# Performance work log

Hardware: AMD Instinct MI355X
Metric: run time of the kernel (lower is better)

## Reference

```python
import jax, jax.numpy as jnp
import numpy as np

INPUT_SIZE = 64
HIDDEN = 1024
SEQ_LEN = 256
BATCH = 128
TARGET_LEN = 96


def lstm_cell(x, h, c, Wih, Whh, bih, bhh):
    # x: [B, in], h/c: [B, H]; torch gate order: i, f, g, o
    z = x @ Wih.T + h @ Whh.T + bih + bhh  # [B, 4H]
    i, f, g, o = jnp.split(z, 4, axis=-1)
    c_new = jax.nn.sigmoid(f) * c + jax.nn.sigmoid(i) * jnp.tanh(g)
    h_new = jax.nn.sigmoid(o) * jnp.tanh(c_new)
    return h_new, c_new


def setup_inputs() -> dict:
    key = jax.random.key(0)
    ks = jax.random.split(key, 12)
    s_in = 1.0 / np.sqrt(HIDDEN)  # torch LSTM init scale ~ U(-1/sqrt(H), 1/sqrt(H))
    def u(k, shape):
        return jax.random.uniform(k, shape, jnp.float32, -s_in, s_in)
    return {
        "input_batch": jax.random.normal(ks[0], (SEQ_LEN, BATCH, INPUT_SIZE), jnp.float32),
        "target_batch": jax.random.normal(ks[1], (TARGET_LEN, BATCH, INPUT_SIZE), jnp.float32),
        "enc_Wih": u(ks[2], (4 * HIDDEN, INPUT_SIZE)),
        "enc_Whh": u(ks[3], (4 * HIDDEN, HIDDEN)),
        "enc_bih": u(ks[4], (4 * HIDDEN,)),
        "enc_bhh": u(ks[5], (4 * HIDDEN,)),
        "dec_Wih": u(ks[6], (4 * HIDDEN, INPUT_SIZE)),
        "dec_Whh": u(ks[7], (4 * HIDDEN, HIDDEN)),
        "dec_bih": u(ks[8], (4 * HIDDEN,)),
        "dec_bhh": u(ks[9], (4 * HIDDEN,)),
        "lin_W": u(ks[10], (INPUT_SIZE, HIDDEN)),
        "lin_b": u(ks[11], (INPUT_SIZE,)),
    }


def reference(input_batch, target_batch, enc_Wih, enc_Whh, enc_bih, enc_bhh,
              dec_Wih, dec_Whh, dec_bih, dec_bhh, lin_W, lin_b):
    B = input_batch.shape[1]
    h0 = jnp.zeros((B, HIDDEN), input_batch.dtype)
    c0 = jnp.zeros((B, HIDDEN), input_batch.dtype)

    # ---- encoder: LSTM over seq_len ----
    def enc_step(carry, x_t):
        h, c = carry
        h, c = lstm_cell(x_t, h, c, enc_Wih, enc_Whh, enc_bih, enc_bhh)
        return (h, c), None
    (h_enc, c_enc), _ = jax.lax.scan(enc_step, (h0, c0), input_batch)

    # ---- decoder: recursive (no teacher forcing), target_len steps ----
    def dec_step(carry, _):
        x, h, c = carry
        h, c = lstm_cell(x, h, c, dec_Wih, dec_Whh, dec_bih, dec_bhh)
        y = h @ lin_W.T + lin_b  # [B, input_size]
        return (y, h, c), y
    x0 = input_batch[-1]  # [B, input_size]
    _, outputs = jax.lax.scan(dec_step, (x0, h_enc, c_enc), None, length=TARGET_LEN)
    return outputs  # [target_len, B, input_size]
```

## Files before the change

### kernel.cpp

```cpp
#include <hip/hip_runtime.h>
#include <stdint.h>

#define IN    64
#define H     1024
#define G4    4096
#define BATCH 128
#define SEQ   256
#define TLEN  96
#define KCAT  1088
#define NSTEP (SEQ + TLEN)
#define NBLK  256
#define HPAD  1032

typedef __attribute__((ext_vector_type(8))) short bf16x8;
typedef __attribute__((ext_vector_type(4))) float f32x4;

__device__ __forceinline__ unsigned short f2bf(float f) {
  union { float f; uint32_t u; } v; v.f = f;
  uint32_t u = v.u;
  return (unsigned short)((u + 0x7fffu + ((u >> 16) & 1u)) >> 16);
}

__device__ __forceinline__ void gload_lds16_sc0(const unsigned short* g, unsigned short* l) {
  __builtin_amdgcn_global_load_lds((const __attribute__((address_space(1))) unsigned int*)g,
                                   (__attribute__((address_space(3))) unsigned int*)l, 16, 0, 1);
}

__global__ void k_convert(const float* __restrict__ src, unsigned short* __restrict__ dst, int n) {
  int i = blockIdx.x * blockDim.x + threadIdx.x;
  int stride = gridDim.x * blockDim.x;
  for (; i < n; i += stride) dst[i] = f2bf(src[i]);
}

__global__ void k_pack(const float* __restrict__ Wih, const float* __restrict__ Whh,
                       const float* __restrict__ bih, const float* __restrict__ bhh,
                       unsigned short* __restrict__ Wcat, float* __restrict__ bcat) {
  int p = blockIdx.x;
  int j = p >> 2, g = p & 3;
  int r = g * H + j;
  for (int c = threadIdx.x; c < KCAT; c += blockDim.x) {
    float v = (c < IN) ? Wih[r * IN + c] : Whh[r * H + (c - IN)];
    Wcat[(size_t)p * KCAT + c] = f2bf(v);
  }
  if (threadIdx.x == 0) bcat[p] = bih[r] + bhh[r];
}

__global__ void k_deceff(const float* __restrict__ Wih, const float* __restrict__ Whh,
                         const float* __restrict__ bih, const float* __restrict__ bhh,
                         const float* __restrict__ lin, const float* __restrict__ linb,
                         unsigned short* __restrict__ Weff, float* __restrict__ beff) {
  int p = blockIdx.x;
  int j = p >> 2, g = p & 3;
  int r = g * H + j;
  __shared__ float wr[IN];
  if (threadIdx.x < IN) wr[threadIdx.x] = Wih[r * IN + threadIdx.x];
  __syncthreads();
  for (int k = threadIdx.x; k < H; k += blockDim.x) {
    float acc = Whh[(size_t)r * H + k];
    #pragma unroll 8
    for (int i = 0; i < IN; ++i) acc += wr[i] * lin[(size_t)i * H + k];
    Weff[(size_t)p * H + k] = f2bf(acc);
  }
  if (threadIdx.x == 0) {
    float s = bih[r] + bhh[r];
    for (int i = 0; i < IN; ++i) s += wr[i] * linb[i];
    beff[p] = s;
  }
}

__global__ __launch_bounds__(512, 2) void k_lstm(
    const unsigned short* __restrict__ xin,
    const unsigned short* __restrict__ Wenc,  const float* __restrict__ benc,
    const unsigned short* __restrict__ Wdec0, const float* __restrict__ bdec0,
    const unsigned short* __restrict__ Wdeff, const float* __restrict__ bdeff,
    unsigned short* __restrict__ hbuf, unsigned short* __restrict__ hhist,
    unsigned int* __restrict__ flags, unsigned int* __restrict__ tickets)
{
  extern __shared__ char smem[];
  unsigned short* hs = (unsigned short*)smem;
  __shared__ unsigned short ht[16][40];
  __shared__ int s_xcd, s_slot;
  const int tid  = threadIdx.x;
  const int lane = tid & 63;
  const int wave = tid >> 6;
  if (tid == 0) {
    unsigned x;
    asm volatile("s_getreg_b32 %0, hwreg(HW_REG_XCC_ID)" : "=s"(x));
    x &= 7;
    unsigned tk = __hip_atomic_fetch_add(&tickets[x], 1u, __ATOMIC_RELAXED, __HIP_MEMORY_SCOPE_AGENT);
    s_xcd = (int)x; s_slot = (int)(tk & 31);
  }
  __syncthreads();
  const int grp  = s_xcd;
  const int slot = s_slot;
  const int m0   = grp * 16;
  const int n0   = slot * 128;
  const int gw   = n0 + wave * 16;
  const int fm   = lane & 15;
  const int fku  = lane >> 4;
  const int fk   = fku * 8;
  const int unit = slot * 32 + wave * 4 + fku;
  const int hrow = tid >> 5;
  const int hcol = tid & 31;
  const unsigned int* myflags = flags + (size_t)grp * 32;

  bf16x8 B[34];
  float4 bias4;
  float cst = 0.f;
  int p = 0;
  for (int t = 0; t < NSTEP; ++t) {
    const bool is_enc = (t < SEQ);
    if (t == 0 || t == SEQ) {
      const unsigned short* W = (t == 0) ? Wenc : Wdec0;
      const unsigned short* wr = W + (size_t)(gw + fm) * KCAT + fk;
      #pragma unroll
      for (int kt = 0; kt < 32; ++kt) B[kt] = *(const bf16x8*)(wr + IN + kt * 32);
      B[32] = *(const bf16x8*)(wr);
      B[33] = *(const bf16x8*)(wr + 32);
    } else if (t == SEQ + 1) {
      const unsigned short* wr = Wdeff + (size_t)(gw + fm) * H + fk;
      #pragma unroll
      for (int kt = 0; kt < 32; ++kt) B[kt] = *(const bf16x8*)(wr + kt * 32);
    }
    if (t == 0 || t == SEQ || t == SEQ + 1) {
      const float* bptr = (t == 0) ? benc : (t == SEQ ? bdec0 : bdeff);
      bias4 = *(const float4*)&bptr[4 * unit];
    }
    const unsigned short* xsrc =
        is_enc ? xin + (size_t)t * BATCH * IN
               : (t == SEQ ? xin + (size_t)(SEQ - 1) * BATCH * IN : nullptr);
    if (t > 0) {
      const unsigned short* hb = hbuf + (size_t)p * BATCH * H + (size_t)m0 * H;
      #pragma unroll
      for (int j = 0; j < 4; ++j) {
        int row  = wave * 2 + (j >> 1);
        int half = (j & 1) * 512;
        gload_lds16_sc0(hb + (size_t)row * H + half + lane * 8, &hs[row * HPAD + half]);
      }
    }
    __syncthreads();
    f32x4 acc0 = {0.f, 0.f, 0.f, 0.f};
    f32x4 acc1 = {0.f, 0.f, 0.f, 0.f};
    if (t > 0) {
      const unsigned short* as = &hs[fm * HPAD + fk];
      #pragma unroll
      for (int kt = 0; kt < 32; kt += 2) {
        acc0 = __builtin_amdgcn_mfma_f32_16x16x32_bf16(B[kt],     *(const bf16x8*)(as + kt * 32),      acc0, 0, 0, 0);
        acc1 = __builtin_amdgcn_mfma_f32_16x16x32_bf16(B[kt + 1], *(const bf16x8*)(as + kt * 32 + 32), acc1, 0, 0, 0);
      }
    }
    if (xsrc) {
      const unsigned short* xa = xsrc + (size_t)(m0 + fm) * IN + fk;
      acc0 = __builtin_amdgcn_mfma_f32_16x16x32_bf16(B[32], *(const bf16x8*)(xa),      acc0, 0, 0, 0);
      acc1 = __builtin_amdgcn_mfma_f32_16x16x32_bf16(B[33], *(const bf16x8*)(xa + 32), acc1, 0, 0, 0);
    }
    {
      float zi = acc0[0] + acc1[0] + bias4.x;
      float zf = acc0[1] + acc1[1] + bias4.y;
      float zg = acc0[2] + acc1[2] + bias4.z;
      float zo = acc0[3] + acc1[3] + bias4.w;
      float gi = 1.f / (1.f + __expf(-zi));
      float gf = 1.f / (1.f + __expf(-zf));
      float gg = tanhf(zg);
      float go = 1.f / (1.f + __expf(-zo));
      float c  = gf * cst + gi * gg;
      cst = c;
      float h = go * tanhf(c);
      ht[fm][(wave << 2) + fku] = f2bf(h);
    }
    __syncthreads();
    {
      unsigned short hv = ht[hrow][hcol];
      size_t idx = (size_t)(m0 + hrow) * H + (size_t)slot * 32 + hcol;
      hbuf[(size_t)(1 - p) * BATCH * H + idx] = hv;
      if (!is_enc) hhist[(size_t)(t - SEQ) * BATCH * H + idx] = hv;
    }
    p ^= 1;
    if (t + 1 < NSTEP) {
      __syncthreads();
      if (tid == 0)
        __hip_atomic_store(&flags[grp * 32 + slot], (unsigned)(t + 1),
                           __ATOMIC_RELAXED, __HIP_MEMORY_SCOPE_AGENT);
      if (tid < 32) {
        while (__hip_atomic_load(&myflags[tid], __ATOMIC_RELAXED, __HIP_MEMORY_SCOPE_AGENT) < (unsigned)(t + 1))
          __builtin_amdgcn_s_sleep(1);
      }
      __syncthreads();
    }
  }
}

__global__ __launch_bounds__(256) void k_out(
    const unsigned short* __restrict__ hhist, const unsigned short* __restrict__ linb16,
    const float* __restrict__ linb, float* __restrict__ out)
{
  const int tid  = threadIdx.x;
  const int lane = tid & 63;
  const int wave = tid >> 6;
  const int fm   = lane & 15;
  const int fk   = (lane >> 4) * 8;
  const int R0   = blockIdx.x * 64 + wave * 16;
  f32x4 acc[4] = {{0.f,0.f,0.f,0.f},{0.f,0.f,0.f,0.f},{0.f,0.f,0.f,0.f},{0.f,0.f,0.f,0.f}};
  const unsigned short* ha = hhist + (size_t)(R0 + fm) * H + fk;
  #pragma unroll 2
  for (int kc = 0; kc < H; kc += 32) {
    bf16x8 a = *(const bf16x8*)(ha + kc);
    #pragma unroll
    for (int nq = 0; nq < 4; ++nq) {
      bf16x8 b = *(const bf16x8*)(linb16 + (size_t)(nq * 16 + fm) * H + fk + kc);
      acc[nq] = __builtin_amdgcn_mfma_f32_16x16x32_bf16(a, b, acc[nq], 0, 0, 0);
    }
  }
  #pragma unroll
  for (int nq = 0; nq < 4; ++nq) {
    int col = nq * 16 + fm;
    float bb = linb[col];
    #pragma unroll
    for (int j = 0; j < 4; ++j) {
      int R = R0 + (lane >> 4) * 4 + j;
      out[(size_t)R * IN + col] = acc[nq][j] + bb;
    }
  }
}

extern "C" void kernel_launch(void* const* d_in, const int* in_sizes, int n_in,
                              void* d_out, int out_size, void* d_ws, size_t ws_size,
                              hipStream_t stream) {
  const float* input_batch = (const float*)d_in[0];
  const float* eWih = (const float*)d_in[2];
  const float* eWhh = (const float*)d_in[3];
  const float* ebih = (const float*)d_in[4];
  const float* ebhh = (const float*)d_in[5];
  const float* dWih = (const float*)d_in[6];
  const float* dWhh = (const float*)d_in[7];
  const float* dbih = (const float*)d_in[8];
  const float* dbhh = (const float*)d_in[9];
  const float* linW = (const float*)d_in[10];
  const float* linb = (const float*)d_in[11];
  float* out = (float*)d_out;

  char* ws = (char*)d_ws;
  size_t off = 0;
  auto alloc = [&](size_t bytes) -> void* {
    void* pp = ws + off;
    off = (off + bytes + 255) & ~(size_t)255;
    return pp;
  };
  unsigned short* xin   = (unsigned short*)alloc((size_t)SEQ * BATCH * IN * 2);
  unsigned short* Wenc  = (unsigned short*)alloc((size_t)G4 * KCAT * 2);
  float*          benc  = (float*)         alloc((size_t)G4 * 4);
  unsigned short* Wdec0 = (unsigned short*)alloc((size_t)G4 * KCAT * 2);
  float*          bdec0 = (float*)         alloc((size_t)G4 * 4);
  unsigned short* Wdeff = (unsigned short*)alloc((size_t)G4 * H * 2);
  float*          bdeff = (float*)         alloc((size_t)G4 * 4);
  unsigned short* linbf = (unsigned short*)alloc((size_t)IN * H * 2);
  unsigned short* hbuf  = (unsigned short*)alloc((size_t)2 * BATCH * H * 2);
  unsigned short* hhist = (unsigned short*)alloc((size_t)TLEN * BATCH * H * 2);
  unsigned int*   flags = (unsigned int*)  alloc((size_t)8 * 32 * sizeof(unsigned));
  unsigned int*   tickets = (unsigned int*)alloc((size_t)8 * sizeof(unsigned));
  (void)ws_size; (void)in_sizes; (void)n_in; (void)out_size;

  hipMemsetAsync(flags, 0, (size_t)8 * 32 * sizeof(unsigned), stream);
  hipMemsetAsync(tickets, 0, (size_t)8 * sizeof(unsigned), stream);
  hipLaunchKernelGGL(k_convert, dim3(512), dim3(256), 0, stream, input_batch, xin, SEQ * BATCH * IN);
  hipLaunchKernelGGL(k_convert, dim3(64),  dim3(256), 0, stream, linW, linbf, IN * H);
  hipLaunchKernelGGL(k_pack,   dim3(G4), dim3(256), 0, stream, eWih, eWhh, ebih, ebhh, Wenc, benc);
  hipLaunchKernelGGL(k_pack,   dim3(G4), dim3(256), 0, stream, dWih, dWhh, dbih, dbhh, Wdec0, bdec0);
  hipLaunchKernelGGL(k_deceff, dim3(G4), dim3(256), 0, stream, dWih, dWhh, dbih, dbhh, linW, linb, Wdeff, bdeff);

  void* args[] = { &xin, &Wenc, &benc, &Wdec0, &bdec0, &Wdeff, &bdeff, &hbuf, &hhist, &flags, &tickets };
  hipLaunchCooperativeKernel((void*)k_lstm, dim3(NBLK), dim3(512), args, 86016, stream);

  hipLaunchKernelGGL(k_out, dim3((TLEN * BATCH) / 64), dim3(256), 0, stream, hhist, linbf, linb, out);
}
```

Before: 3.984 ms.

## Replace per-step group barrier with per-slice flag waits, restructure LDS layout, fast tanh

The full barrier at the end of each step, where 32 lanes spun on every peer's flag, is removed. Each wave now waits only on the flags of the four hidden-state slices it loads and issues each slice's LDS load as soon as that producer is ready. The LDS layout of the hidden-state tile changes from padded row-major to per-slice MFMA-fragment order, and the x operand loads are hoisted ahead of the h loads. tanhf is replaced with an exp-based fast_tanh. The finer-grained sync lets waiting overlap with loading, but it must still keep the double buffer in hbuf safe from overwrite, and fast_tanh slightly changes numerics.

```diff
diff --git a/kernel.cpp b/kernel.cpp
--- a/kernel.cpp
+++ b/kernel.cpp
@@ -10,7 +10,6 @@
 #define KCAT  1088
 #define NSTEP (SEQ + TLEN)
 #define NBLK  256
-#define HPAD  1032
 
 typedef __attribute__((ext_vector_type(8))) short bf16x8;
 typedef __attribute__((ext_vector_type(4))) float f32x4;
@@ -19,6 +18,13 @@
   union { float f; uint32_t u; } v; v.f = f;
   uint32_t u = v.u;
   return (unsigned short)((u + 0x7fffu + ((u >> 16) & 1u)) >> 16);
+}
+
+__device__ __forceinline__ float fast_tanh(float x) {
+  float ax = fabsf(x);
+  float e  = __expf(-2.f * ax);
+  float r  = (1.f - e) / (1.f + e);
+  return copysignf(r, x);
 }
 
 __device__ __forceinline__ void gload_lds16_sc0(const unsigned short* g, unsigned short* l) {
@@ -94,15 +100,14 @@
   const int grp  = s_xcd;
   const int slot = s_slot;
   const int m0   = grp * 16;
-  const int n0   = slot * 128;
-  const int gw   = n0 + wave * 16;
+  const int gw   = slot * 128 + wave * 16;
   const int fm   = lane & 15;
   const int fku  = lane >> 4;
   const int fk   = fku * 8;
   const int unit = slot * 32 + wave * 4 + fku;
   const int hrow = tid >> 5;
   const int hcol = tid & 31;
-  const unsigned int* myflags = flags + (size_t)grp * 32;
+  unsigned int* gflags = flags + (size_t)grp * 32;
 
   bf16x8 B[34];
   float4 bias4;
@@ -126,33 +131,38 @@
       const float* bptr = (t == 0) ? benc : (t == SEQ ? bdec0 : bdeff);
       bias4 = *(const float4*)&bptr[4 * unit];
     }
-    const unsigned short* xsrc =
-        is_enc ? xin + (size_t)t * BATCH * IN
-               : (t == SEQ ? xin + (size_t)(SEQ - 1) * BATCH * IN : nullptr);
+    const bool hasx = is_enc || (t == SEQ);
+    bf16x8 xa0, xa1;
+    if (hasx) {
+      const unsigned short* xsrc = xin + (size_t)(is_enc ? t : SEQ - 1) * BATCH * IN;
+      const unsigned short* xa = xsrc + (size_t)(m0 + fm) * IN + fk;
+      xa0 = *(const bf16x8*)(xa);
+      xa1 = *(const bf16x8*)(xa + 32);
+    }
     if (t > 0) {
       const unsigned short* hb = hbuf + (size_t)p * BATCH * H + (size_t)m0 * H;
       #pragma unroll
       for (int j = 0; j < 4; ++j) {
-        int row  = wave * 2 + (j >> 1);
-        int half = (j & 1) * 512;
-        gload_lds16_sc0(hb + (size_t)row * H + half + lane * 8, &hs[row * HPAD + half]);
+        const int s = wave * 4 + j;
+        while (__hip_atomic_load(&gflags[s], __ATOMIC_RELAXED, __HIP_MEMORY_SCOPE_AGENT) < (unsigned)t)
+          __builtin_amdgcn_s_sleep(1);
+        gload_lds16_sc0(hb + (size_t)fm * H + s * 32 + fk, &hs[s * 512]);
       }
     }
     __syncthreads();
     f32x4 acc0 = {0.f, 0.f, 0.f, 0.f};
     f32x4 acc1 = {0.f, 0.f, 0.f, 0.f};
     if (t > 0) {
-      const unsigned short* as = &hs[fm * HPAD + fk];
+      const unsigned short* as = &hs[fku * 128 + fm * 8];
       #pragma unroll
       for (int kt = 0; kt < 32; kt += 2) {
-        acc0 = __builtin_amdgcn_mfma_f32_16x16x32_bf16(B[kt],     *(const bf16x8*)(as + kt * 32),      acc0, 0, 0, 0);
-        acc1 = __builtin_amdgcn_mfma_f32_16x16x32_bf16(B[kt + 1], *(const bf16x8*)(as + kt * 32 + 32), acc1, 0, 0, 0);
+        acc0 = __builtin_amdgcn_mfma_f32_16x16x32_bf16(B[kt],     *(const bf16x8*)(as + kt * 512),       acc0, 0, 0, 0);
+        acc1 = __builtin_amdgcn_mfma_f32_16x16x32_bf16(B[kt + 1], *(const bf16x8*)(as + kt * 512 + 512), acc1, 0, 0, 0);
       }
     }
-    if (xsrc) {
-      const unsigned short* xa = xsrc + (size_t)(m0 + fm) * IN + fk;
-      acc0 = __builtin_amdgcn_mfma_f32_16x16x32_bf16(B[32], *(const bf16x8*)(xa),      acc0, 0, 0, 0);
-      acc1 = __builtin_amdgcn_mfma_f32_16x16x32_bf16(B[33], *(const bf16x8*)(xa + 32), acc1, 0, 0, 0);
+    if (hasx) {
+      acc0 = __builtin_amdgcn_mfma_f32_16x16x32_bf16(B[32], xa0, acc0, 0, 0, 0);
+      acc1 = __builtin_amdgcn_mfma_f32_16x16x32_bf16(B[33], xa1, acc1, 0, 0, 0);
     }
     {
       float zi = acc0[0] + acc1[0] + bias4.x;
@@ -161,11 +171,11 @@
       float zo = acc0[3] + acc1[3] + bias4.w;
       float gi = 1.f / (1.f + __expf(-zi));
       float gf = 1.f / (1.f + __expf(-zf));
-      float gg = tanhf(zg);
+      float gg = fast_tanh(zg);
       float go = 1.f / (1.f + __expf(-zo));
       float c  = gf * cst + gi * gg;
       cst = c;
-      float h = go * tanhf(c);
+      float h = go * fast_tanh(c);
       ht[fm][(wave << 2) + fku] = f2bf(h);
     }
     __syncthreads();
@@ -179,13 +189,8 @@
     if (t + 1 < NSTEP) {
       __syncthreads();
       if (tid == 0)
-        __hip_atomic_store(&flags[grp * 32 + slot], (unsigned)(t + 1),
+        __hip_atomic_store(&gflags[slot], (unsigned)(t + 1),
                            __ATOMIC_RELAXED, __HIP_MEMORY_SCOPE_AGENT);
-      if (tid < 32) {
-        while (__hip_atomic_load(&myflags[tid], __ATOMIC_RELAXED, __HIP_MEMORY_SCOPE_AGENT) < (unsigned)(t + 1))
-          __builtin_amdgcn_s_sleep(1);
-      }
-      __syncthreads();
     }
   }
 }
```

Result: slower. 4.360 ms (+9.4%).
